# Performance work log

Hardware: AMD Instinct MI355X
Metric: run time of the kernel (lower is better)

## Reference

```python
import jax, jax.numpy as jnp
import numpy as np

LAYERS, DIM, FFN, HEADS = 2, 1024, 4096, 8
HD = DIM // HEADS          # head qk dim = 128
VD = DIM                   # v_dim (double_v_dim=False)
HV = VD // HEADS           # head v dim = 128
B, L = 2, 2048
SCALE_BASE = 512.0
EPS = 1e-5


def setup_inputs() -> dict:
    key = jax.random.key(0)
    ks = jax.random.split(key, 18)
    def rn(k, shape, s=1.0):
        return jax.random.normal(k, shape, dtype=jnp.float32) * s
    return dict(
        X=rn(ks[0], (B, L, DIM)),
        Wq=rn(ks[1], (LAYERS, HEADS, DIM, HD), 1.0 / DIM),
        Wk=rn(ks[2], (LAYERS, HEADS, DIM, HD), 1.0 / DIM),
        Wv=rn(ks[3], (LAYERS, HEADS, DIM, HV), 1.0 / DIM),
        W_G=rn(ks[4], (LAYERS, DIM, VD), 1.0 / DIM),
        W_O=rn(ks[5], (LAYERS, VD, DIM), 1.0 / DIM),
        gn_w=1.0 + 0.02 * rn(ks[6], (LAYERS, VD)),
        gn_b=0.02 * rn(ks[7], (LAYERS, VD)),
        ln1_w=1.0 + 0.02 * rn(ks[8], (LAYERS, DIM)),
        ln1_b=0.02 * rn(ks[9], (LAYERS, DIM)),
        ln2_w=1.0 + 0.02 * rn(ks[10], (LAYERS, DIM)),
        ln2_b=0.02 * rn(ks[11], (LAYERS, DIM)),
        ffn_w1=rn(ks[12], (LAYERS, DIM, FFN), DIM ** -0.5),
        ffn_b1=0.02 * rn(ks[13], (LAYERS, FFN)),
        ffn_w2=rn(ks[14], (LAYERS, FFN, DIM), FFN ** -0.5),
        ffn_b2=0.02 * rn(ks[15], (LAYERS, DIM)),
    )


def _xpos_tables(length, head_dim):
    half = head_dim // 2
    pos = jnp.arange(length, dtype=jnp.float32)
    base_scale = (jnp.arange(0, head_dim, 2, dtype=jnp.float32) + 0.4 * head_dim) / (1.4 * head_dim)
    sc = base_scale[None, :] ** (pos / SCALE_BASE)[:, None]          # [L, half]
    inv_freq = 1.0 / (10000.0 ** (jnp.arange(half, dtype=jnp.float32) / half))
    ang = pos[:, None] * inv_freq[None, :]                           # [L, half]
    return sc, jnp.sin(ang), jnp.cos(ang)


def _dup(t):
    # duplicate_interleave: [L, half] -> [L, head_dim]
    return jnp.repeat(t, 2, axis=-1)


def _rotate_every_two(x):
    x1, x2 = x[..., ::2], x[..., 1::2]
    return jnp.stack([-x2, x1], axis=-1).reshape(x.shape)


def _apply_xpos(x, sc, sin, cos, downscale):
    s = 1.0 / sc if downscale else sc
    return x * _dup(cos * s) + _rotate_every_two(x) * _dup(sin * s)


def _layernorm(x, w, b):
    mu = jnp.mean(x, axis=-1, keepdims=True)
    var = jnp.var(x, axis=-1, keepdims=True)
    return (x - mu) * jax.lax.rsqrt(var + EPS) * w + b


def _decay_matrix(length):
    gammas = jnp.asarray(1.0 - np.exp(np.linspace(np.log(1 / 32), np.log(1 / 512), HEADS)), dtype=jnp.float32)
    n = jnp.arange(length, dtype=jnp.float32)
    delta = n[:, None] - n[None, :]                                  # [L, L]
    logg = jnp.log(gammas)[:, None, None]                            # [H, 1, 1]
    return jnp.where(delta[None] >= 0, jnp.exp(logg * delta[None]), 0.0)  # [H, L, L]


def _msr(X, Wq, Wk, Wv, gn_w, gn_b, W_G, W_O, D, sc, sin, cos):
    b, l, d = X.shape
    Q = _apply_xpos(jnp.einsum('bld,hde->bhle', X, Wq), sc, sin, cos, False)
    K = _apply_xpos(jnp.einsum('bld,hde->bhle', X, Wk), sc, sin, cos, True)
    V = jnp.einsum('bld,hdv->bhlv', X, Wv)
    scores = jnp.einsum('bhle,bhme->bhlm', Q, K) * D[None]           # [B,H,L,L] decayed
    Y = jnp.einsum('bhlm,bhmv->bhlv', scores, V)                     # [B,H,L,HV]
    # GroupNorm(heads, v_dim) over per-token concatenated heads == per-head norm
    mu = jnp.mean(Y, axis=-1, keepdims=True)
    var = jnp.var(Y, axis=-1, keepdims=True)
    Yn = (Y - mu) * jax.lax.rsqrt(var + EPS)
    Yn = Yn * gn_w.reshape(HEADS, 1, HV)[None] + gn_b.reshape(HEADS, 1, HV)[None]
    Yc = jnp.transpose(Yn, (0, 2, 1, 3)).reshape(b, l, VD)
    G = X @ W_G
    gate = G * jax.nn.sigmoid(G)                                     # swish
    return (gate * Yc) @ W_O


def reference(X, Wq, Wk, Wv, W_G, W_O, gn_w, gn_b, ln1_w, ln1_b, ln2_w, ln2_b, ffn_w1, ffn_b1, ffn_w2, ffn_b2):
    l = X.shape[1]
    sc, sin, cos = _xpos_tables(l, HD)
    D = _decay_matrix(l)
    for i in range(LAYERS):
        Y = _msr(_layernorm(X, ln1_w[i], ln1_b[i]), Wq[i], Wk[i], Wv[i],
                 gn_w[i], gn_b[i], W_G[i], W_O[i], D, sc, sin, cos) + X
        h = _layernorm(Y, ln2_w[i], ln2_b[i])
        h = jax.nn.gelu(h @ ffn_w1[i] + ffn_b1[i], approximate=False)
        X = h @ ffn_w2[i] + ffn_b2[i] + Y                            # Dropout is identity in eval
    return X
```

## Files before the change

### kernel.cpp

```cpp
#include <hip/hip_runtime.h>
#include <math.h>

#define DIM 1024
#define FFN_DIM 4096
#define HEADS 8
#define HD 128
#define BB 2
#define LL 2048
#define NROWS (BB*LL)

typedef __attribute__((ext_vector_type(8))) short bf16x8;
typedef __attribute__((ext_vector_type(4))) short bf16x4;
typedef __attribute__((ext_vector_type(2))) short bf16x2;
typedef __attribute__((ext_vector_type(4))) float f32x4;

__device__ inline short f2bf(float f) {
    unsigned u = __builtin_bit_cast(unsigned, f);
    unsigned r = (u + 0x7FFFu + ((u >> 16) & 1u)) >> 16;
    return (short)r;
}
__device__ inline float bf2f(short s) {
    unsigned u = ((unsigned)(unsigned short)s) << 16;
    return __builtin_bit_cast(float, u);
}

__device__ __forceinline__ void gl_lds16(const void* g, void* l) {
    __builtin_amdgcn_global_load_lds(
        (const __attribute__((address_space(1))) unsigned int*)g,
        (__attribute__((address_space(3))) unsigned int*)l, 16, 0, 0);
}

__global__ __launch_bounds__(256) void ln_kernel_bf(
    const float* __restrict__ x, const float* __restrict__ w,
    const float* __restrict__ b, short* __restrict__ out)
{
    int row = blockIdx.x;
    int tid = threadIdx.x;
    const float* xr = x + (size_t)row * DIM;
    float4 v = *(const float4*)(xr + tid * 4);
    float s  = v.x + v.y + v.z + v.w;
    float ss = v.x*v.x + v.y*v.y + v.z*v.z + v.w*v.w;
    #pragma unroll
    for (int o = 32; o > 0; o >>= 1) { s += __shfl_down(s, o); ss += __shfl_down(ss, o); }
    __shared__ float red[10];
    int wid = tid >> 6;
    if ((tid & 63) == 0) { red[wid] = s; red[4 + wid] = ss; }
    __syncthreads();
    if (tid == 0) {
        float t  = red[0] + red[1] + red[2] + red[3];
        float t2 = red[4] + red[5] + red[6] + red[7];
        float mu  = t * (1.f / DIM);
        float var = t2 * (1.f / DIM) - mu * mu;
        red[8] = mu; red[9] = rsqrtf(var + 1e-5f);
    }
    __syncthreads();
    float mu = red[8], rs = red[9];
    float4 wv = *(const float4*)(w + tid * 4);
    float4 bv = *(const float4*)(b + tid * 4);
    bf16x4 o;
    o[0] = f2bf((v.x - mu) * rs * wv.x + bv.x);
    o[1] = f2bf((v.y - mu) * rs * wv.y + bv.y);
    o[2] = f2bf((v.z - mu) * rs * wv.z + bv.z);
    o[3] = f2bf((v.w - mu) * rs * wv.w + bv.w);
    *(bf16x4*)(out + (size_t)row * DIM + tid * 4) = o;
}

__global__ __launch_bounds__(256) void transpose_cvt(
    const float* __restrict__ in, short* __restrict__ out,
    int R, int C, size_t ibs, size_t obs)
{
    __shared__ float t[32][33];
    int bz = blockIdx.z;
    int r0 = blockIdx.y * 32, c0 = blockIdx.x * 32;
    int tx = threadIdx.x & 31, ty = threadIdx.x >> 5;
    const float* ip = in + (size_t)bz * ibs;
    short* op = out + (size_t)bz * obs;
    #pragma unroll
    for (int i = 0; i < 4; ++i)
        t[ty + i * 8][tx] = ip[(size_t)(r0 + ty + i * 8) * C + c0 + tx];
    __syncthreads();
    #pragma unroll
    for (int i = 0; i < 4; ++i)
        op[(size_t)(c0 + ty + i * 8) * R + r0 + tx] = f2bf(t[tx][ty + i * 8]);
}

__global__ __launch_bounds__(256) void vt_cvt(
    const short* __restrict__ Vb, short* __restrict__ Vt)
{
    __shared__ short t[32][34];
    int r0 = blockIdx.y * 32, c0 = blockIdx.x * 32;
    int tx = threadIdx.x & 31, ty = threadIdx.x >> 5;
    #pragma unroll
    for (int i = 0; i < 4; ++i)
        t[ty + i * 8][tx] = Vb[(size_t)(r0 + ty + i * 8) * DIM + c0 + tx];
    __syncthreads();
    int b = r0 >> 11;
    int l = (r0 & (LL - 1));
    #pragma unroll
    for (int i = 0; i < 4; ++i) {
        int c = c0 + ty + i * 8;
        int h = c >> 7, v = c & 127;
        Vt[(((size_t)(b * HEADS + h) * HD + v) << 11) + l + tx] = t[tx][ty + i * 8];
    }
}

template<int EPI, int MI, int NI, int GX>
__global__ __launch_bounds__(512, 2) void gemm_pipe(
    const short* __restrict__ A, const short* __restrict__ Bt,
    void* __restrict__ Cv, const float* __restrict__ bias,
    const float* __restrict__ R_,
    void* __restrict__ P1, void* __restrict__ P2, void* __restrict__ P3,
    int N, int K, int M)
{
    constexpr int BM = 32 * MI;
    constexpr int BN = 64 * NI;
    constexpr int LA = BM / 64;
    constexpr int LB = BN / 64;
    __shared__ __align__(16) short As[2][BM * 64];
    __shared__ __align__(16) short Bs[2][BN * 64];
    int tid = threadIdx.x;
    int w = tid >> 6, lane = tid & 63;
    int q = lane >> 4, lr = lane & 15;
    int wr = w >> 2, wc = w & 3;

    int id = blockIdx.y * GX + blockIdx.x;
    int xcd = id & 7, j = id >> 3;
    constexpr int rx_n = (GX >= 8) ? GX / 8 : 1;
    int tp = (GX * gridDim.y) >> 3;
    int rh = tp >> 3;
    int lbx = j & 7, lby = j >> 3;
    int rx = xcd % rx_n, ry = xcd / rx_n;
    int bm = (ry * rh + lby) * BM;
    int bn = (rx * 8 + lbx) * BN;

    int srow = tid >> 3;
    int sseg = tid & 7;

    f32x4 acc[MI][NI];
    #pragma unroll
    for (int mi = 0; mi < MI; ++mi)
        #pragma unroll
        for (int ni = 0; ni < NI; ++ni) acc[mi][ni] = (f32x4){0.f, 0.f, 0.f, 0.f};

    auto stageA = [&](int bb, int k0) {
        #pragma unroll
        for (int i = 0; i < LA; ++i) {
            int row = i * 64 + srow;
            gl_lds16(A + (size_t)(bm + row) * K + k0 + ((sseg ^ (row & 7)) << 3),
                     &As[bb][(i * 512 + tid) * 8]);
        }
    };
    auto stageB = [&](int bb, int k0) {
        #pragma unroll
        for (int i = 0; i < LB; ++i) {
            int row = i * 64 + srow;
            gl_lds16(Bt + (size_t)(bn + row) * K + k0 + ((sseg ^ (row & 7)) << 3),
                     &Bs[bb][(i * 512 + tid) * 8]);
        }
    };

    stageA(0, 0);
    stageB(0, 0);

    int aoff = (wr * (BM / 2) + lr) * 64;
    int boff = (wc * (BN / 4) + lr) * 64;
    int seg0 = ((q ^ (lr & 7)) << 3);
    int seg1 = (((4 + q) ^ (lr & 7)) << 3);

    int nk = K >> 6;
    #pragma unroll 1
    for (int kt = 0; kt < nk; ++kt) {
        int b = kt & 1;
        if (kt + 1 < nk) {
            stageA(b ^ 1, (kt + 1) << 6);
            if constexpr (LA == 4)
                asm volatile("s_waitcnt vmcnt(4)\ns_barrier" ::: "memory");
            else
                asm volatile("s_waitcnt vmcnt(2)\ns_barrier" ::: "memory");
        } else {
            asm volatile("s_waitcnt vmcnt(0)\ns_barrier" ::: "memory");
        }
        const short* as = As[b];
        const short* bs = Bs[b];
        bf16x8 af[MI], bfr[NI];
        #pragma unroll
        for (int mi = 0; mi < MI; ++mi)
            af[mi] = *(const bf16x8*)&as[aoff + mi * 1024 + seg0];
        #pragma unroll
        for (int ni = 0; ni < NI; ++ni)
            bfr[ni] = *(const bf16x8*)&bs[boff + ni * 1024 + seg0];
        __builtin_amdgcn_s_setprio(1);
        #pragma unroll
        for (int mi = 0; mi < MI; ++mi)
            #pragma unroll
            for (int ni = 0; ni < NI; ++ni)
                acc[mi][ni] = __builtin_amdgcn_mfma_f32_16x16x32_bf16(af[mi], bfr[ni], acc[mi][ni], 0, 0, 0);
        __builtin_amdgcn_s_setprio(0);
        if (kt + 1 < nk) stageB(b ^ 1, (kt + 1) << 6);
        #pragma unroll
        for (int mi = 0; mi < MI; ++mi)
            af[mi] = *(const bf16x8*)&as[aoff + mi * 1024 + seg1];
        #pragma unroll
        for (int ni = 0; ni < NI; ++ni)
            bfr[ni] = *(const bf16x8*)&bs[boff + ni * 1024 + seg1];
        __builtin_amdgcn_s_setprio(1);
        #pragma unroll
        for (int mi = 0; mi < MI; ++mi)
            #pragma unroll
            for (int ni = 0; ni < NI; ++ni)
                acc[mi][ni] = __builtin_amdgcn_mfma_f32_16x16x32_bf16(af[mi], bfr[ni], acc[mi][ni], 0, 0, 0);
        __builtin_amdgcn_s_setprio(0);
        asm volatile("s_barrier" ::: "memory");
    }

    if constexpr (EPI == 4) {
        int sel = bn >> 10;
        int row_base = bm + wr * (BM / 2) + q * 4;
        int l0 = row_base & (LL - 1);
        #pragma unroll
        for (int ni = 0; ni < NI; ++ni) {
            int col = bn + wc * (BN / 4) + ni * 16 + lr;
            int cq = col & (DIM - 1);
            if (sel <= 1) {
                int jj = (col & 127) >> 1;
                float lb = log2f((2.f * jj + 51.2f) / 179.2f);
                if (sel == 1) lb = -lb;
                float invf = exp2f(-(float)jj * (13.287712379549449f / 64.f));
                float snb, cnb;
                sincosf((float)l0 * invf, &snb, &cnb);
                float scb = exp2f(lb * (float)l0 * (1.f / 512.f));
                float s1, c1, s16, c16;
                __sincosf(invf, &s1, &c1);
                __sincosf(16.f * invf, &s16, &c16);
                float st1 = exp2f(lb * (1.f / 512.f));
                float st16 = exp2f(lb * (16.f / 512.f));
                short* Ob = (short*)(sel == 0 ? Cv : P1);
                #pragma unroll
                for (int mi = 0; mi < MI; ++mi) {
                    float cr = cnb, sr = snb, sv = scb;
                    #pragma unroll
                    for (int r = 0; r < 4; ++r) {
                        float cs = cr * sv, ssn = sr * sv;
                        float v = acc[mi][ni][r];
                        float p = __shfl_xor(v, 1);
                        float o = (lr & 1) ? (v * cs + p * ssn) : (v * cs - p * ssn);
                        Ob[(size_t)(row_base + mi * 16 + r) * DIM + cq] = f2bf(o);
                        if (r < 3) {
                            float crn = cr * c1 - sr * s1;
                            sr = sr * c1 + cr * s1; cr = crn;
                            sv *= st1;
                        }
                    }
                    float cbn = cnb * c16 - snb * s16;
                    snb = snb * c16 + cnb * s16; cnb = cbn;
                    scb *= st16;
                }
            } else if (sel == 2) {
                short* Vb = (short*)P2;
                #pragma unroll
                for (int mi = 0; mi < MI; ++mi)
                    #pragma unroll
                    for (int r = 0; r < 4; ++r)
                        Vb[(size_t)(row_base + mi * 16 + r) * DIM + cq] = f2bf(acc[mi][ni][r]);
            } else {
                short* Gb = (short*)P3;
                #pragma unroll
                for (int mi = 0; mi < MI; ++mi)
                    #pragma unroll
                    for (int r = 0; r < 4; ++r)
                        Gb[(size_t)(row_base + mi * 16 + r) * DIM + cq] = f2bf(acc[mi][ni][r]);
            }
        }
        return;
    }

    float* Cf = (float*)Cv;
    short* Cs = (short*)Cv;
    #pragma unroll
    for (int ni = 0; ni < NI; ++ni) {
        int col = bn + wc * (BN / 4) + ni * 16 + lr;
        float bi = 0.f;
        if constexpr (EPI == 1 || EPI == 2) bi = bias[col];
        #pragma unroll
        for (int mi = 0; mi < MI; ++mi) {
            int row0 = bm + wr * (BM / 2) + mi * 16 + q * 4;
            #pragma unroll
            for (int r = 0; r < 4; ++r) {
                size_t off = (size_t)(row0 + r) * M + col;
                float v = acc[mi][ni][r];
                if constexpr (EPI == 1) {
                    v += bi;
                    v = 0.5f * v * (1.f + erff(v * 0.70710678118654752f));
                    Cs[off] = f2bf(v);
                } else if constexpr (EPI == 2) {
                    Cf[off] = v + bi + R_[off];
                } else if constexpr (EPI == 3) {
                    Cf[off] = v + R_[off];
                } else {
                    Cf[off] = v;
                }
            }
        }
    }
}

#define PSTR 40
__global__ __launch_bounds__(512, 2) void retention_mfma2(
    const short* __restrict__ Qb, const short* __restrict__ Kb,
    const short* __restrict__ Vt, float* __restrict__ Y)
{
    __shared__ __align__(16) short Ks[2][64 * 128];
    __shared__ __align__(16) short Vs[2][128 * 64];
    __shared__ __align__(16) short Ps[8][16 * PSTR];
    int tid = threadIdx.x;
    int w = tid >> 6, lane = tid & 63;
    int q = lane >> 4, lr = lane & 15;
    int g = w >> 2;
    int qw = w & 3;
    int bh = blockIdx.x;
    int b = bh >> 3, h = bh & 7;
    size_t bL = (size_t)b * LL;
    const short* Kbh = Kb + (bL << 10) + (h << 7);
    const short* Qbh = Qb + (bL << 10) + (h << 7);
    const short* Vbh = Vt + ((size_t)bh << 18);
    float* Ybh = Y + (bL << 10) + (h << 7);

    const float lg_lo = -3.4657359027997265f;
    const float lg_hi = -6.2383246250395075f;
    float gamma = 1.f - expf(lg_lo + (lg_hi - lg_lo) * ((float)h / 7.f));
    float logg = logf(gamma);
    float gm64 = expf(-64.f * logg);
    float rf[4];
    #pragma unroll
    for (int r = 0; r < 4; ++r) rf[r] = expf(logg * (float)(q * 4 + r));
    float cf0 = expf(-logg * (float)lr);
    float cf1 = expf(-logg * (float)(16 + lr));
    int dqlr = q * 4 - lr;

    int kr_l = lane >> 4;
    int ks_l = lane & 15;
    int vr_l = lane >> 3;
    int vs_l = lane & 7;

    auto stageKV = [&](int bb, int m0) {
        #pragma unroll
        for (int i = 0; i < 2; ++i) {
            int ch = w * 2 + i;
            int kr = ch * 4 + kr_l;
            gl_lds16(Kbh + ((size_t)(m0 + kr) << 10) + ((ks_l ^ (kr & 15)) << 3),
                     &Ks[bb][ch * 512]);
            int vr = ch * 8 + vr_l;
            gl_lds16(Vbh + ((size_t)vr << 11) + m0 + ((vs_l ^ (vr & 7)) << 3),
                     &Vs[bb][ch * 512]);
        }
    };

    #pragma unroll 1
    for (int pass = 0; pass < 2; ++pass) {
        int jt = pass ? (31 - blockIdx.y) : blockIdx.y;
        int l0w = jt * 64 + qw * 16;
        int ns = jt + 1;

        bf16x8 qf[4];
        {
            const short* qp = Qbh + ((size_t)(l0w + lr) << 10) + q * 8;
            #pragma unroll
            for (int es = 0; es < 4; ++es) qf[es] = *(const bf16x8*)(qp + es * 32);
        }
        f32x4 yacc[8];
        #pragma unroll
        for (int vt = 0; vt < 8; ++vt) yacc[vt] = (f32x4){0.f, 0.f, 0.f, 0.f};
        float tf = expf(logg * (float)(l0w - g * 32));

        stageKV(0, 0);

        #pragma unroll 1
        for (int s = 0; s < ns; ++s) {
            int buf = s & 1;
            if (s + 1 < ns) {
                stageKV(buf ^ 1, (s + 1) * 64);
                asm volatile("s_waitcnt vmcnt(4)\ns_barrier" ::: "memory");
            } else {
                asm volatile("s_waitcnt vmcnt(0)\ns_barrier" ::: "memory");
            }
            int m0 = s * 64 + g * 32;
            if (m0 <= l0w + 15) {
                int dt = l0w - m0;
                const short* ksub = &Ks[buf][g * 32 * 128];
                f32x4 sa0 = (f32x4){0.f,0.f,0.f,0.f};
                f32x4 sa1 = (f32x4){0.f,0.f,0.f,0.f};
                #pragma unroll
                for (int es = 0; es < 4; ++es) {
                    int slot = ((es * 4 + q) ^ lr) * 8;
                    bf16x8 bk0 = *(const bf16x8*)&ksub[lr * 128 + slot];
                    bf16x8 bk1 = *(const bf16x8*)&ksub[(16 + lr) * 128 + slot];
                    sa0 = __builtin_amdgcn_mfma_f32_16x16x32_bf16(qf[es], bk0, sa0, 0, 0, 0);
                    sa1 = __builtin_amdgcn_mfma_f32_16x16x32_bf16(qf[es], bk1, sa1, 0, 0, 0);
                }
                #pragma unroll
                for (int r = 0; r < 4; ++r) {
                    float p0 = sa0[r] * (rf[r] * cf0 * tf);
                    float p1 = sa1[r] * (rf[r] * cf1 * tf);
                    int d0 = dt + dqlr + r;
                    Ps[w][(q*4 + r) * PSTR + lr]      = (d0 >= 0)      ? f2bf(p0) : (short)0;
                    Ps[w][(q*4 + r) * PSTR + 16 + lr] = (d0 - 16 >= 0) ? f2bf(p1) : (short)0;
                }
                bf16x8 pa = *(const bf16x8*)&Ps[w][lr * PSTR + q * 8];
                #pragma unroll
                for (int vt = 0; vt < 8; ++vt) {
                    bf16x8 bv = *(const bf16x8*)&Vs[buf][(vt * 16 + lr) * 64 + (((g * 4 + q) ^ (lr & 7)) << 3)];
                    yacc[vt] = __builtin_amdgcn_mfma_f32_16x16x32_bf16(pa, bv, yacc[vt], 0, 0, 0);
                }
            }
            tf *= gm64;
            asm volatile("s_barrier" ::: "memory");
        }
        __syncthreads();
        float* sc = (float*)&Ks[0][0] + qw * 2048;
        if (g) {
            #pragma unroll
            for (int vt = 0; vt < 8; ++vt)
                #pragma unroll
                for (int r = 0; r < 4; ++r)
                    sc[(q * 4 + r) * 128 + ((vt * 16 + lr) ^ (q * 8))] = yacc[vt][r];
        }
        __syncthreads();
        if (!g) {
            float* yp = Ybh + ((size_t)(l0w + q * 4) << 10) + lr;
            #pragma unroll
            for (int vt = 0; vt < 8; ++vt)
                #pragma unroll
                for (int r = 0; r < 4; ++r)
                    yp[((size_t)r << 10) + vt * 16] =
                        yacc[vt][r] + sc[(q * 4 + r) * 128 + ((vt * 16 + lr) ^ (q * 8))];
        }
        __syncthreads();
    }
}

__global__ __launch_bounds__(256) void gn_gate_kernel(
    const float* __restrict__ Y, const short* __restrict__ Gb,
    const float* __restrict__ w, const float* __restrict__ b,
    short* __restrict__ ybf)
{
    int tid = threadIdx.x;
    int wid = tid >> 6, lane = tid & 63;
    int grp = blockIdx.x * 4 + wid;
    int n = grp >> 3, h = grp & 7;
    size_t base = (size_t)n * DIM + h * HD + lane * 2;
    float2 y = *(const float2*)(Y + base);
    float s = y.x + y.y, ss = y.x * y.x + y.y * y.y;
    #pragma unroll
    for (int o = 32; o > 0; o >>= 1) { s += __shfl_down(s, o); ss += __shfl_down(ss, o); }
    s = __shfl(s, 0); ss = __shfl(ss, 0);
    float mu  = s * (1.f / HD);
    float var = ss * (1.f / HD) - mu * mu;
    float rs  = rsqrtf(var + 1e-5f);
    float2 wv = *(const float2*)(w + h * HD + lane * 2);
    float2 bv = *(const float2*)(b + h * HD + lane * 2);
    bf16x2 gv = *(const bf16x2*)(Gb + base);
    float gx = bf2f(gv[0]), gy = bf2f(gv[1]);
    float g0 = gx / (1.f + expf(-gx));
    float g1 = gy / (1.f + expf(-gy));
    bf16x2 o;
    o[0] = f2bf(((y.x - mu) * rs * wv.x + bv.x) * g0);
    o[1] = f2bf(((y.y - mu) * rs * wv.y + bv.y) * g1);
    *(bf16x2*)(ybf + base) = o;
}

extern "C" void kernel_launch(void* const* d_in, const int* in_sizes, int n_in,
                              void* d_out, int out_size, void* d_ws, size_t ws_size,
                              hipStream_t stream)
{
    const float* X0   = (const float*)d_in[0];
    const float* Wq   = (const float*)d_in[1];
    const float* Wk   = (const float*)d_in[2];
    const float* Wv   = (const float*)d_in[3];
    const float* WG   = (const float*)d_in[4];
    const float* WO   = (const float*)d_in[5];
    const float* gnw  = (const float*)d_in[6];
    const float* gnb  = (const float*)d_in[7];
    const float* ln1w = (const float*)d_in[8];
    const float* ln1b = (const float*)d_in[9];
    const float* ln2w = (const float*)d_in[10];
    const float* ln2b = (const float*)d_in[11];
    const float* fw1  = (const float*)d_in[12];
    const float* fb1  = (const float*)d_in[13];
    const float* fw2  = (const float*)d_in[14];
    const float* fb2  = (const float*)d_in[15];

    float* ws = (float*)d_ws;
    const size_t U = (size_t)NROWS * DIM;

    short* lnbf  = (short*)(ws + 0 * U);
    short* wqkvg = lnbf + (size_t)NROWS * DIM;
    short* Vt   = (short*)(ws + 1 * U);
    short* fw1t = (short*)(ws + 1 * U);
    short* fw2t = fw1t + (size_t)DIM * FFN_DIM;
    float* sY  = ws + 2 * U;
    short* h1   = (short*)(ws + 2 * U);
    short* Vb   = (short*)(ws + 3 * U);
    short* ybf  = (short*)(ws + 3 * U);
    short* wot  = ybf + (size_t)NROWS * DIM;
    short* Gb   = (short*)(ws + 4 * U);
    float* sXn = ws + 4 * U;
    short* Qb   = (short*)(ws + 5 * U);
    short* Kb   = Qb + (size_t)NROWS * DIM;
    float* sX  = ws + 6 * U;

    for (int i = 0; i < 2; ++i) {
        const float* Xin = (i == 0) ? X0 : sX;
        float* Xout = (i == 1) ? (float*)d_out : sX;

        ln_kernel_bf<<<NROWS, 256, 0, stream>>>(Xin, ln1w + i * DIM, ln1b + i * DIM, lnbf);
        dim3 tq(HD / 32, DIM / 32, HEADS);
        transpose_cvt<<<tq, 256, 0, stream>>>(Wq + (size_t)i * HEADS * DIM * HD, wqkvg + 0 * DIM * DIM, DIM, HD, (size_t)DIM * HD, (size_t)HD * DIM);
        transpose_cvt<<<tq, 256, 0, stream>>>(Wk + (size_t)i * HEADS * DIM * HD, wqkvg + 1 * DIM * DIM, DIM, HD, (size_t)DIM * HD, (size_t)HD * DIM);
        transpose_cvt<<<tq, 256, 0, stream>>>(Wv + (size_t)i * HEADS * DIM * HD, wqkvg + 2 * DIM * DIM, DIM, HD, (size_t)DIM * HD, (size_t)HD * DIM);
        dim3 tg(DIM / 32, DIM / 32, 1);
        transpose_cvt<<<tg, 256, 0, stream>>>(WG + (size_t)i * DIM * DIM, wqkvg + 3 * (size_t)DIM * DIM, DIM, DIM, 0, 0);
        dim3 gp4(4 * DIM / 256, NROWS / 256);
        gemm_pipe<4, 8, 4, 16><<<gp4, 512, 0, stream>>>(lnbf, wqkvg, Qb, nullptr, nullptr, Kb, Vb, Gb, NROWS, DIM, 4 * DIM);
        dim3 vg(DIM / 32, NROWS / 32);
        vt_cvt<<<vg, 256, 0, stream>>>(Vb, Vt);
        dim3 rg(16, 16);
        retention_mfma2<<<rg, 512, 0, stream>>>(Qb, Kb, Vt, sY);
        gn_gate_kernel<<<NROWS * HEADS / 4, 256, 0, stream>>>(sY, Gb, gnw + i * DIM, gnb + i * DIM, ybf);
        transpose_cvt<<<tg, 256, 0, stream>>>(WO + (size_t)i * DIM * DIM, wot, DIM, DIM, 0, 0);
        dim3 gp(DIM / 128, NROWS / 128);
        gemm_pipe<3, 4, 2, 8><<<gp, 512, 0, stream>>>(ybf, wot, sXn, nullptr, Xin, nullptr, nullptr, nullptr, NROWS, DIM, DIM);
        ln_kernel_bf<<<NROWS, 256, 0, stream>>>(sXn, ln2w + i * DIM, ln2b + i * DIM, lnbf);
        dim3 t1(FFN_DIM / 32, DIM / 32, 1);
        transpose_cvt<<<t1, 256, 0, stream>>>(fw1 + (size_t)i * DIM * FFN_DIM, fw1t, DIM, FFN_DIM, 0, 0);
        dim3 t2(DIM / 32, FFN_DIM / 32, 1);
        transpose_cvt<<<t2, 256, 0, stream>>>(fw2 + (size_t)i * FFN_DIM * DIM, fw2t, FFN_DIM, DIM, 0, 0);
        dim3 gf1(FFN_DIM / 256, NROWS / 256);
        gemm_pipe<1, 8, 4, 16><<<gf1, 512, 0, stream>>>(lnbf, fw1t, h1, fb1 + i * FFN_DIM, nullptr, nullptr, nullptr, nullptr, NROWS, DIM, FFN_DIM);
        dim3 gf2(DIM / 128, NROWS / 128);
        gemm_pipe<2, 4, 2, 8><<<gf2, 512, 0, stream>>>(h1, fw2t, Xout, fb2 + i * DIM, sXn, nullptr, nullptr, nullptr, NROWS, FFN_DIM, DIM);
    }
}
```

Before: 747.4 us.

## Deepen GEMM LDS pipeline to four stages for MI=4 tile configs

For GEMM instantiations with MI==4, the kernel now keeps four LDS buffers and prefetches three k-tiles ahead, replacing the two-stage double buffer. The waitcnt values are tuned to the number of loads still outstanding. The goal is to hide more global-load latency behind MFMA work. The cost is that LDS use per block roughly doubles, which likely lowers how many blocks can be resident per CU. The MMA inner body is moved into a shared lambda.

Measured after the change: 723.4 us. -3.2%, faster.

```diff
diff --git a/kernel.cpp b/kernel.cpp
--- a/kernel.cpp
+++ b/kernel.cpp
@@ -116,8 +116,9 @@
     constexpr int BN = 64 * NI;
     constexpr int LA = BM / 64;
     constexpr int LB = BN / 64;
-    __shared__ __align__(16) short As[2][BM * 64];
-    __shared__ __align__(16) short Bs[2][BN * 64];
+    constexpr int NBUF = (MI == 4) ? 4 : 2;
+    __shared__ __align__(16) short As[NBUF][BM * 64];
+    __shared__ __align__(16) short Bs[NBUF][BN * 64];
     int tid = threadIdx.x;
     int w = tid >> 6, lane = tid & 63;
     int q = lane >> 4, lr = lane & 15;
@@ -159,36 +160,19 @@
         }
     };
 
-    stageA(0, 0);
-    stageB(0, 0);
-
     int aoff = (wr * (BM / 2) + lr) * 64;
     int boff = (wc * (BN / 4) + lr) * 64;
     int seg0 = ((q ^ (lr & 7)) << 3);
     int seg1 = (((4 + q) ^ (lr & 7)) << 3);
 
-    int nk = K >> 6;
-    #pragma unroll 1
-    for (int kt = 0; kt < nk; ++kt) {
-        int b = kt & 1;
-        if (kt + 1 < nk) {
-            stageA(b ^ 1, (kt + 1) << 6);
-            if constexpr (LA == 4)
-                asm volatile("s_waitcnt vmcnt(4)\ns_barrier" ::: "memory");
-            else
-                asm volatile("s_waitcnt vmcnt(2)\ns_barrier" ::: "memory");
-        } else {
-            asm volatile("s_waitcnt vmcnt(0)\ns_barrier" ::: "memory");
-        }
-        const short* as = As[b];
-        const short* bs = Bs[b];
+    auto compute_half = [&](const short* as, const short* bs, int seg) {
         bf16x8 af[MI], bfr[NI];
         #pragma unroll
         for (int mi = 0; mi < MI; ++mi)
-            af[mi] = *(const bf16x8*)&as[aoff + mi * 1024 + seg0];
+            af[mi] = *(const bf16x8*)&as[aoff + mi * 1024 + seg];
         #pragma unroll
         for (int ni = 0; ni < NI; ++ni)
-            bfr[ni] = *(const bf16x8*)&bs[boff + ni * 1024 + seg0];
+            bfr[ni] = *(const bf16x8*)&bs[boff + ni * 1024 + seg];
         __builtin_amdgcn_s_setprio(1);
         #pragma unroll
         for (int mi = 0; mi < MI; ++mi)
@@ -196,21 +180,53 @@
             for (int ni = 0; ni < NI; ++ni)
                 acc[mi][ni] = __builtin_amdgcn_mfma_f32_16x16x32_bf16(af[mi], bfr[ni], acc[mi][ni], 0, 0, 0);
         __builtin_amdgcn_s_setprio(0);
-        if (kt + 1 < nk) stageB(b ^ 1, (kt + 1) << 6);
-        #pragma unroll
-        for (int mi = 0; mi < MI; ++mi)
-            af[mi] = *(const bf16x8*)&as[aoff + mi * 1024 + seg1];
-        #pragma unroll
-        for (int ni = 0; ni < NI; ++ni)
-            bfr[ni] = *(const bf16x8*)&bs[boff + ni * 1024 + seg1];
-        __builtin_amdgcn_s_setprio(1);
-        #pragma unroll
-        for (int mi = 0; mi < MI; ++mi)
-            #pragma unroll
-            for (int ni = 0; ni < NI; ++ni)
-                acc[mi][ni] = __builtin_amdgcn_mfma_f32_16x16x32_bf16(af[mi], bfr[ni], acc[mi][ni], 0, 0, 0);
-        __builtin_amdgcn_s_setprio(0);
-        asm volatile("s_barrier" ::: "memory");
+    };
+
+    int nk = K >> 6;
+
+    if constexpr (NBUF == 2) {
+        stageA(0, 0);
+        stageB(0, 0);
+        #pragma unroll 1
+        for (int kt = 0; kt < nk; ++kt) {
+            int b = kt & 1;
+            if (kt + 1 < nk) {
+                stageA(b ^ 1, (kt + 1) << 6);
+                if constexpr (LA == 4)
+                    asm volatile("s_waitcnt vmcnt(4)\ns_barrier" ::: "memory");
+                else
+                    asm volatile("s_waitcnt vmcnt(2)\ns_barrier" ::: "memory");
+            } else {
+                asm volatile("s_waitcnt vmcnt(0)\ns_barrier" ::: "memory");
+            }
+            compute_half(As[b], Bs[b], seg0);
+            if (kt + 1 < nk) stageB(b ^ 1, (kt + 1) << 6);
+            compute_half(As[b], Bs[b], seg1);
+            asm volatile("s_barrier" ::: "memory");
+        }
+    } else {
+        #pragma unroll
+        for (int d = 0; d < 3; ++d) {
+            stageA(d, d << 6);
+            stageB(d, d << 6);
+        }
+        #pragma unroll 1
+        for (int kt = 0; kt < nk; ++kt) {
+            int b = kt & 3;
+            if (kt + 3 < nk) {
+                int bb = (kt + 3) & 3;
+                stageA(bb, (kt + 3) << 6);
+                stageB(bb, (kt + 3) << 6);
+            }
+            int rem = nk - 1 - kt;
+            if (rem >= 3)      asm volatile("s_waitcnt vmcnt(12)\ns_barrier" ::: "memory");
+            else if (rem == 2) asm volatile("s_waitcnt vmcnt(8)\ns_barrier" ::: "memory");
+            else if (rem == 1) asm volatile("s_waitcnt vmcnt(4)\ns_barrier" ::: "memory");
+            else               asm volatile("s_waitcnt vmcnt(0)\ns_barrier" ::: "memory");
+            compute_half(As[b], Bs[b], seg0);
+            compute_half(As[b], Bs[b], seg1);
+            asm volatile("s_barrier" ::: "memory");
+        }
     }
 
     if constexpr (EPI == 4) {
```
